# Optimization experiments

Measured on AMD Instinct MI355X. Metric: run time of the kernel, lower is better.

Reference implementation:

```python
import jax, jax.numpy as jnp
import numpy as np
from itertools import combinations

Nt, Nrf, Nk, FEAT, BATCH = 64, 4, 8, 512, 1024
Ng = Nt // Nk                      # 8
_MAX = len(list(combinations(range(Ng), Nrf)))  # 70
CSETSIZE = int(2 ** np.floor(np.log2(_MAX)))    # 64
SQRT_NRF = np.float32(np.sqrt(Nrf))


def _generate_antenna_selection_set(num_target):
    """Max-hamming-distance antenna selection set (numpy, matches torch code)."""
    combs = list(combinations(range(Ng), Nrf))
    maxSize = len(combs)
    globalSet = np.zeros((maxSize, Nt, Nrf), np.float32)
    for i, act in enumerate(combs):
        for j, a in enumerate(act):
            globalSet[i, a * Nk:a * Nk + Nk, j] = 1.0
    gsum = globalSet.sum(-1)  # (maxSize, Nt)
    selectSet = np.zeros((num_target, Nt, Nrf), np.float32)
    available = []
    for idx in range(num_target):
        if len(available) == 0:
            available = list(range(maxSize))
        if idx == 0:
            hd = np.zeros(len(available))
        else:
            sel = selectSet[:idx].sum(-1)            # (idx, Nt)
            cand = gsum[np.array(available)]          # (nAvail, Nt)
            hd = (sel[None, :, :] != cand[:, None, :]).sum(axis=(1, 2))
        sid = available[int(np.argmax(hd))]
        selectSet[idx] = globalSet[sid]
        available.remove(sid)
    return selectSet


def setup_inputs() -> dict:
    key = jax.random.key(0)
    ks = jax.random.split(key, 7)
    s = 1.0 / np.sqrt(FEAT)
    DDIM = CSETSIZE * Nrf * Nrf
    return {
        "x": jax.random.normal(ks[0], (BATCH, FEAT), jnp.float32),
        "W_A": jax.random.normal(ks[1], (Nt, FEAT), jnp.float32) * s,
        "b_A": jax.random.normal(ks[2], (Nt,), jnp.float32) * s,
        "W_Dr": jax.random.normal(ks[3], (DDIM, FEAT), jnp.float32) * s,
        "b_Dr": jax.random.normal(ks[4], (DDIM,), jnp.float32) * s,
        "W_Di": jax.random.normal(ks[5], (DDIM, FEAT), jnp.float32) * s,
        "b_Di": jax.random.normal(ks[6], (DDIM,), jnp.float32) * s,
        "CSet": jnp.asarray(_generate_antenna_selection_set(CSETSIZE)),
    }


def reference(x, W_A, b_A, W_Dr, b_Dr, W_Di, b_Di, CSet):
    B = x.shape[0]
    theta = x @ W_A.T + b_A                          # (B, Nt)
    cosT, sinT = jnp.cos(theta), jnp.sin(theta)
    eye = jnp.eye(Nt, dtype=x.dtype)
    A_real = (cosT[:, :, None] * eye)[:, None]       # (B, 1, Nt, Nt) diag-embed
    A_imag = (sinT[:, :, None] * eye)[:, None]
    D_real = (x @ W_Dr.T + b_Dr).reshape(B, CSETSIZE, Nrf, Nrf)
    D_imag = (x @ W_Di.T + b_Di).reshape(B, CSETSIZE, Nrf, Nrf)
    # diag(cos) @ C == row-scale of C (identical math to the dense matmul)
    ArC = cosT[:, None, :, None] * CSet[None]        # (B, CSetSize, Nt, Nrf)
    AiC = sinT[:, None, :, None] * CSet[None]
    ArCDr = ArC @ D_real
    ArCDi = ArC @ D_imag
    AiCDr = AiC @ D_real
    AiCDi = AiC @ D_imag
    V_real = ArCDr - AiCDi                           # (B, CSetSize, Nt, Nrf)
    V_imag = ArCDi + AiCDr
    V_F = jnp.sqrt(jnp.sum(V_real ** 2 + V_imag ** 2, axis=(2, 3)))
    V_F = V_F[:, :, None, None]
    D_real_n = SQRT_NRF * D_real / V_F
    D_imag_n = SQRT_NRF * D_imag / V_F
    return (A_real, A_imag, D_real_n, D_imag_n, CSet)
```

## Files before the change

kernel.cpp:

```cpp
#include <hip/hip_runtime.h>
#include <math.h>

#define BATCH 1024
#define FEAT  512
#define NT    64
#define DDIM  1024

typedef __attribute__((ext_vector_type(8))) short  short8;
typedef __attribute__((ext_vector_type(4))) float  floatx4;

#define AIMG_OFF  0
#define BIMG_OFF  1048576
#define THETA_OFF 3276800

__device__ __forceinline__ unsigned short bf16rne(float f) {
    unsigned int u = __float_as_uint(f);
    return (unsigned short)((u + 0x7fffu + ((u >> 16) & 1u)) >> 16);
}

__device__ __forceinline__ void gld16(const unsigned char* g, unsigned char* l) {
    __builtin_amdgcn_global_load_lds(
        (const __attribute__((address_space(1))) unsigned int*)g,
        (__attribute__((address_space(3))) unsigned int*)l, 16, 0, 0);
}

__global__ __launch_bounds__(256) void k0_convert(
    const float* __restrict__ x,
    const float* __restrict__ W_A,
    const float* __restrict__ W_Dr,
    const float* __restrict__ W_Di,
    unsigned char* __restrict__ ws)
{
    unsigned short* aimg = (unsigned short*)(ws + AIMG_OFF);
    unsigned short* bimg = (unsigned short*)(ws + BIMG_OFF);
    const int gtid = blockIdx.x * 256 + threadIdx.x;

    for (int idx = gtid; idx < 200704; idx += 65536) {
        const float* src;
        unsigned short* dst;
        if (idx < 65536) {
            const int rt = idx >> 12, kb = (idx >> 9) & 7;
            const int r  = (idx >> 3) & 63, c = idx & 7;
            src = x + ((size_t)(rt * 64 + r) * FEAT + kb * 64 + c * 8);
            dst = aimg + ((rt * 8 + kb) * 4096 + r * 64 + ((c ^ (r & 7)) * 8));
        } else {
            const int j  = idx - 65536;
            const int ct = j >> 12, kb = (j >> 9) & 7;
            const int n  = (j >> 3) & 63, c = j & 7;
            const float* wrow;
            if (ct < 32) {
                const int g = n >> 5, h = (n >> 4) & 1, pos = n & 15;
                wrow = (h ? W_Di : W_Dr) + (size_t)(ct * 32 + g * 16 + pos) * FEAT;
            } else {
                wrow = W_A + (size_t)n * FEAT;
            }
            src = wrow + kb * 64 + c * 8;
            dst = bimg + ((ct * 8 + kb) * 4096 + n * 64 + ((c ^ (n & 7)) * 8));
        }
        const float4 v0 = *(const float4*)src;
        const float4 v1 = *(const float4*)(src + 4);
        short8 o;
        o[0] = (short)bf16rne(v0.x); o[1] = (short)bf16rne(v0.y);
        o[2] = (short)bf16rne(v0.z); o[3] = (short)bf16rne(v0.w);
        o[4] = (short)bf16rne(v1.x); o[5] = (short)bf16rne(v1.y);
        o[6] = (short)bf16rne(v1.z); o[7] = (short)bf16rne(v1.w);
        *(short8*)dst = o;
    }
}

__global__ __launch_bounds__(256) void k1_gemm(
    const unsigned char* __restrict__ ws,
    const float* __restrict__ b_A,
    const float* __restrict__ b_Dr, const float* __restrict__ b_Di,
    float* __restrict__ out, float* __restrict__ theta_ws)
{
    __shared__ __align__(16) unsigned char smem[32768];

    const int bid  = blockIdx.x;
    const int rt   = bid & 15;
    const int ct   = bid >> 4;
    const int tid  = threadIdx.x;
    const int lane = tid & 63;
    const int wv   = tid >> 6;
    const int ln   = lane & 15;
    const int quad = lane >> 4;
    const int row0 = rt * 64;

    const unsigned char* Atiles = ws + AIMG_OFF + (size_t)rt * 8 * 8192;
    const unsigned char* Btiles = ws + BIMG_OFF + (size_t)ct * 8 * 8192;

    const int g0 = (wv * 2 + 0) * 1024;
    const int g1 = (wv * 2 + 1) * 1024;
    const int lo = lane * 16;

    floatx4 acc[4] = {{0,0,0,0},{0,0,0,0},{0,0,0,0},{0,0,0,0}};

    {
        unsigned char* La = smem;
        unsigned char* Lb = smem + 8192;
        gld16(Atiles + g0 + lo, La + g0);
        gld16(Atiles + g1 + lo, La + g1);
        gld16(Btiles + g0 + lo, Lb + g0);
        gld16(Btiles + g1 + lo, Lb + g1);
    }

    const int rowOffA = (wv * 16 + ln) * 128;
    const int swz = ln & 7;
    int cur = 0;

    #pragma unroll 1
    for (int kb = 0; kb < 8; ++kb) {
        __syncthreads();
        if (kb < 7) {
            const unsigned char* At = Atiles + (kb + 1) * 8192;
            const unsigned char* Bt = Btiles + (kb + 1) * 8192;
            unsigned char* La = smem + (cur ^ 1) * 16384;
            unsigned char* Lb = La + 8192;
            gld16(At + g0 + lo, La + g0);
            gld16(At + g1 + lo, La + g1);
            gld16(Bt + g0 + lo, Lb + g0);
            gld16(Bt + g1 + lo, Lb + g1);
        }
        const unsigned char* La = smem + cur * 16384;
        const unsigned char* Lb = La + 8192;
        #pragma unroll
        for (int ks = 0; ks < 2; ++ks) {
            const int ca = ((ks * 4 + quad) ^ swz) * 16;
            const short8 a = *(const short8*)(La + rowOffA + ca);
            #pragma unroll
            for (int t = 0; t < 4; ++t) {
                const short8 b = *(const short8*)(Lb + (t * 16 + ln) * 128 + ca);
                acc[t] = __builtin_amdgcn_mfma_f32_16x16x32_bf16(a, b, acc[t], 0, 0, 0);
            }
        }
        cur ^= 1;
    }

    if (ct < 32) {
        const size_t drn = (size_t)2 * BATCH * 4096;
        const size_t din = drn + (size_t)BATCH * DDIM;
        const int woff = ct * 32;
        #pragma unroll
        for (int p = 0; p < 2; ++p) {
            const int colg = woff + p * 16 + ln;
            const float br = b_Dr[colg];
            const float bi = b_Di[colg];
            float dr[4], di[4], ps[4];
            #pragma unroll
            for (int i = 0; i < 4; ++i) {
                dr[i] = acc[2 * p][i] + br;
                di[i] = acc[2 * p + 1][i] + bi;
                ps[i] = dr[i] * dr[i] + di[i] * di[i];
            }
            #pragma unroll
            for (int i = 0; i < 4; ++i) {
                ps[i] += __shfl_xor(ps[i], 1);
                ps[i] += __shfl_xor(ps[i], 2);
                ps[i] += __shfl_xor(ps[i], 4);
                ps[i] += __shfl_xor(ps[i], 8);
            }
            #pragma unroll
            for (int i = 0; i < 4; ++i) {
                const float scale = 2.0f / sqrtf(8.0f * ps[i]);
                const size_t row_g = (size_t)(row0 + wv * 16 + quad * 4 + i);
                out[drn + row_g * DDIM + colg] = dr[i] * scale;
                out[din + row_g * DDIM + colg] = di[i] * scale;
            }
        }
    } else {
        #pragma unroll
        for (int t = 0; t < 4; ++t) {
            const int colg = t * 16 + ln;
            const float ba = b_A[colg];
            #pragma unroll
            for (int i = 0; i < 4; ++i) {
                const int row_g = row0 + wv * 16 + quad * 4 + i;
                theta_ws[row_g * NT + colg] = acc[t][i] + ba;
            }
        }
    }
}

__global__ __launch_bounds__(256) void k2_fill(
    const float* __restrict__ theta_ws,
    const float* __restrict__ cset,
    float* __restrict__ out)
{
    const int beta = blockIdx.x;
    const int tid  = threadIdx.x;

    if (beta < 4096) {
        const int b  = beta >> 2;
        const int rg = beta & 3;
        const int t  = rg * 16 + (tid >> 4);
        const int j  = tid & 15;

        const float th = theta_ws[b * NT + t];
        float s, c;
        sincosf(th, &s, &c);

        float4 vr = {0.f, 0.f, 0.f, 0.f};
        float4 vi = {0.f, 0.f, 0.f, 0.f};
        if ((t >> 2) == j) {
            ((float*)&vr)[t & 3] = c;
            ((float*)&vi)[t & 3] = s;
        }
        const size_t off = (size_t)b * 4096 + t * 64 + j * 4;
        *(float4*)(out + off) = vr;
        *(float4*)(out + (size_t)BATCH * 4096 + off) = vi;
    } else {
        const int cb = beta - 4096;
        const size_t base = (size_t)2 * BATCH * 4096 + (size_t)2 * BATCH * DDIM;
        ((float4*)(out + base))[cb * 256 + tid] = ((const float4*)cset)[cb * 256 + tid];
    }
}

extern "C" void kernel_launch(void* const* d_in, const int* in_sizes, int n_in,
                              void* d_out, int out_size, void* d_ws, size_t ws_size,
                              hipStream_t stream) {
    const float* x    = (const float*)d_in[0];
    const float* W_A  = (const float*)d_in[1];
    const float* b_A  = (const float*)d_in[2];
    const float* W_Dr = (const float*)d_in[3];
    const float* b_Dr = (const float*)d_in[4];
    const float* W_Di = (const float*)d_in[5];
    const float* b_Di = (const float*)d_in[6];
    const float* CSet = (const float*)d_in[7];
    float* out = (float*)d_out;
    unsigned char* ws = (unsigned char*)d_ws;
    float* theta = (float*)(ws + THETA_OFF);

    k0_convert<<<256, 256, 0, stream>>>(x, W_A, W_Dr, W_Di, ws);
    k1_gemm<<<528, 256, 0, stream>>>(ws, b_A, b_Dr, b_Di, out, theta);
    k2_fill<<<4112, 256, 0, stream>>>(theta, CSet, out);
}
```

Baseline: 107.1 us.

## Merge three launches into two, computing theta in prep kernel and A fill in GEMM

The theta GEMM (x·W_A) moves out of the main GEMM kernel into dedicated blocks of the prep kernel, which convert x and W_A to bf16 on the fly through LDS. The CSet copy also moves into the prep kernel. The diagonal A_real/A_imag fill becomes extra blocks of the main GEMM kernel, one block per batch row with sincos computed once into shared memory. This cuts one kernel launch and its inter-kernel gap, and lets the output fill overlap with the D GEMM, at the cost of an unpipelined small GEMM sitting in the prep kernel.

After: 109.6 us. +2.4%, slower.

```diff
diff --git a/kernel.cpp b/kernel.cpp
--- a/kernel.cpp
+++ b/kernel.cpp
@@ -7,6 +7,7 @@
 #define DDIM  1024
 
 typedef __attribute__((ext_vector_type(8))) short  short8;
+typedef __attribute__((ext_vector_type(4))) short  short4v;
 typedef __attribute__((ext_vector_type(4))) float  floatx4;
 
 #define AIMG_OFF  0
@@ -16,6 +17,12 @@
 __device__ __forceinline__ unsigned short bf16rne(float f) {
     unsigned int u = __float_as_uint(f);
     return (unsigned short)((u + 0x7fffu + ((u >> 16) & 1u)) >> 16);
+}
+__device__ __forceinline__ short4v pack4(const float4 a) {
+    short4v r;
+    r[0] = (short)bf16rne(a.x); r[1] = (short)bf16rne(a.y);
+    r[2] = (short)bf16rne(a.z); r[3] = (short)bf16rne(a.w);
+    return r;
 }
 
 __device__ __forceinline__ void gld16(const unsigned char* g, unsigned char* l) {
@@ -24,119 +31,181 @@
         (__attribute__((address_space(3))) unsigned int*)l, 16, 0, 0);
 }
 
-__global__ __launch_bounds__(256) void k0_convert(
+
+__global__ __launch_bounds__(256) void k0_prep(
     const float* __restrict__ x,
-    const float* __restrict__ W_A,
-    const float* __restrict__ W_Dr,
-    const float* __restrict__ W_Di,
-    unsigned char* __restrict__ ws)
+    const float* __restrict__ W_A,  const float* __restrict__ b_A,
+    const float* __restrict__ W_Dr, const float* __restrict__ W_Di,
+    const float* __restrict__ cset,
+    unsigned char* __restrict__ ws, float* __restrict__ out)
 {
-    unsigned short* aimg = (unsigned short*)(ws + AIMG_OFF);
-    unsigned short* bimg = (unsigned short*)(ws + BIMG_OFF);
-    const int gtid = blockIdx.x * 256 + threadIdx.x;
-
-    for (int idx = gtid; idx < 200704; idx += 65536) {
-        const float* src;
-        unsigned short* dst;
-        if (idx < 65536) {
-            const int rt = idx >> 12, kb = (idx >> 9) & 7;
-            const int r  = (idx >> 3) & 63, c = idx & 7;
-            src = x + ((size_t)(rt * 64 + r) * FEAT + kb * 64 + c * 8);
-            dst = aimg + ((rt * 8 + kb) * 4096 + r * 64 + ((c ^ (r & 7)) * 8));
-        } else {
-            const int j  = idx - 65536;
-            const int ct = j >> 12, kb = (j >> 9) & 7;
-            const int n  = (j >> 3) & 63, c = j & 7;
-            const float* wrow;
-            if (ct < 32) {
+    __shared__ __align__(16) unsigned short As[64][40];
+    __shared__ __align__(16) unsigned short Bs[64][40];
+
+    const int bid = blockIdx.x;
+    const int tid = threadIdx.x;
+
+    if (bid < 256) {
+        unsigned short* aimg = (unsigned short*)(ws + AIMG_OFF);
+        unsigned short* bimg = (unsigned short*)(ws + BIMG_OFF);
+        const int gtid = bid * 256 + tid;
+        for (int idx = gtid; idx < 196608; idx += 65536) {
+            const float* src;
+            unsigned short* dst;
+            if (idx < 65536) {
+                const int rt = idx >> 12, kb = (idx >> 9) & 7;
+                const int r  = (idx >> 3) & 63, c = idx & 7;
+                src = x + ((size_t)(rt * 64 + r) * FEAT + kb * 64 + c * 8);
+                dst = aimg + ((rt * 8 + kb) * 4096 + r * 64 + ((c ^ (r & 7)) * 8));
+            } else {
+                const int j  = idx - 65536;
+                const int ct = j >> 12, kb = (j >> 9) & 7;
+                const int n  = (j >> 3) & 63, c = j & 7;
                 const int g = n >> 5, h = (n >> 4) & 1, pos = n & 15;
-                wrow = (h ? W_Di : W_Dr) + (size_t)(ct * 32 + g * 16 + pos) * FEAT;
-            } else {
-                wrow = W_A + (size_t)n * FEAT;
-            }
-            src = wrow + kb * 64 + c * 8;
-            dst = bimg + ((ct * 8 + kb) * 4096 + n * 64 + ((c ^ (n & 7)) * 8));
-        }
-        const float4 v0 = *(const float4*)src;
-        const float4 v1 = *(const float4*)(src + 4);
-        short8 o;
-        o[0] = (short)bf16rne(v0.x); o[1] = (short)bf16rne(v0.y);
-        o[2] = (short)bf16rne(v0.z); o[3] = (short)bf16rne(v0.w);
-        o[4] = (short)bf16rne(v1.x); o[5] = (short)bf16rne(v1.y);
-        o[6] = (short)bf16rne(v1.z); o[7] = (short)bf16rne(v1.w);
-        *(short8*)dst = o;
+                const float* wrow =
+                    (h ? W_Di : W_Dr) + (size_t)(ct * 32 + g * 16 + pos) * FEAT;
+                src = wrow + kb * 64 + c * 8;
+                dst = bimg + ((ct * 8 + kb) * 4096 + n * 64 + ((c ^ (n & 7)) * 8));
+            }
+            const float4 v0 = *(const float4*)src;
+            const float4 v1 = *(const float4*)(src + 4);
+            short8 o;
+            o[0] = (short)bf16rne(v0.x); o[1] = (short)bf16rne(v0.y);
+            o[2] = (short)bf16rne(v0.z); o[3] = (short)bf16rne(v0.w);
+            o[4] = (short)bf16rne(v1.x); o[5] = (short)bf16rne(v1.y);
+            o[6] = (short)bf16rne(v1.z); o[7] = (short)bf16rne(v1.w);
+            *(short8*)dst = o;
+        }
+    } else if (bid < 272) {
+        float* theta_ws = (float*)(ws + THETA_OFF);
+        const int lane = tid & 63;
+        const int wv   = tid >> 6;
+        const int ln   = lane & 15;
+        const int quad = lane >> 4;
+        const int f = tid & 7;
+        const int r = tid >> 3;
+        const int row0 = (bid - 256) * 64;
+
+        const float* arow0 = x + (size_t)(row0 + r) * FEAT;
+        const float* arow1 = x + (size_t)(row0 + r + 32) * FEAT;
+        const float* brow0 = W_A + (size_t)r * FEAT;
+        const float* brow1 = W_A + (size_t)(r + 32) * FEAT;
+
+        float4 pa0 = *(const float4*)(arow0 + f * 4);
+        float4 pa1 = *(const float4*)(arow1 + f * 4);
+        float4 pb0 = *(const float4*)(brow0 + f * 4);
+        float4 pb1 = *(const float4*)(brow1 + f * 4);
+
+        floatx4 acc[4] = {{0,0,0,0},{0,0,0,0},{0,0,0,0},{0,0,0,0}};
+
+        #pragma unroll 1
+        for (int it = 0; it < 16; ++it) {
+            __syncthreads();
+            *(short4v*)&As[r][f * 4]      = pack4(pa0);
+            *(short4v*)&As[r + 32][f * 4] = pack4(pa1);
+            *(short4v*)&Bs[r][f * 4]      = pack4(pb0);
+            *(short4v*)&Bs[r + 32][f * 4] = pack4(pb1);
+            __syncthreads();
+            if (it < 15) {
+                const int ko = (it + 1) * 32 + f * 4;
+                pa0 = *(const float4*)(arow0 + ko);
+                pa1 = *(const float4*)(arow1 + ko);
+                pb0 = *(const float4*)(brow0 + ko);
+                pb1 = *(const float4*)(brow1 + ko);
+            }
+            const short8 a = *(const short8*)&As[wv * 16 + ln][quad * 8];
+            #pragma unroll
+            for (int t = 0; t < 4; ++t) {
+                const short8 b = *(const short8*)&Bs[t * 16 + ln][quad * 8];
+                acc[t] = __builtin_amdgcn_mfma_f32_16x16x32_bf16(a, b, acc[t], 0, 0, 0);
+            }
+        }
+        #pragma unroll
+        for (int t = 0; t < 4; ++t) {
+            const int colg = t * 16 + ln;
+            const float ba = b_A[colg];
+            #pragma unroll
+            for (int i = 0; i < 4; ++i) {
+                const int row_g = row0 + wv * 16 + quad * 4 + i;
+                theta_ws[row_g * NT + colg] = acc[t][i] + ba;
+            }
+        }
+    } else {
+        const int cb = bid - 272;
+        const size_t base = (size_t)2 * BATCH * 4096 + (size_t)2 * BATCH * DDIM;
+        ((float4*)(out + base))[cb * 256 + tid] = ((const float4*)cset)[cb * 256 + tid];
     }
 }
 
-__global__ __launch_bounds__(256) void k1_gemm(
+__global__ __launch_bounds__(256) void k1_main(
     const unsigned char* __restrict__ ws,
-    const float* __restrict__ b_A,
     const float* __restrict__ b_Dr, const float* __restrict__ b_Di,
-    float* __restrict__ out, float* __restrict__ theta_ws)
+    float* __restrict__ out)
 {
     __shared__ __align__(16) unsigned char smem[32768];
 
-    const int bid  = blockIdx.x;
-    const int rt   = bid & 15;
-    const int ct   = bid >> 4;
-    const int tid  = threadIdx.x;
-    const int lane = tid & 63;
-    const int wv   = tid >> 6;
-    const int ln   = lane & 15;
-    const int quad = lane >> 4;
-    const int row0 = rt * 64;
-
-    const unsigned char* Atiles = ws + AIMG_OFF + (size_t)rt * 8 * 8192;
-    const unsigned char* Btiles = ws + BIMG_OFF + (size_t)ct * 8 * 8192;
-
-    const int g0 = (wv * 2 + 0) * 1024;
-    const int g1 = (wv * 2 + 1) * 1024;
-    const int lo = lane * 16;
-
-    floatx4 acc[4] = {{0,0,0,0},{0,0,0,0},{0,0,0,0},{0,0,0,0}};
-
-    {
-        unsigned char* La = smem;
-        unsigned char* Lb = smem + 8192;
-        gld16(Atiles + g0 + lo, La + g0);
-        gld16(Atiles + g1 + lo, La + g1);
-        gld16(Btiles + g0 + lo, Lb + g0);
-        gld16(Btiles + g1 + lo, Lb + g1);
-    }
-
-    const int rowOffA = (wv * 16 + ln) * 128;
-    const int swz = ln & 7;
-    int cur = 0;
-
-    #pragma unroll 1
-    for (int kb = 0; kb < 8; ++kb) {
-        __syncthreads();
-        if (kb < 7) {
-            const unsigned char* At = Atiles + (kb + 1) * 8192;
-            const unsigned char* Bt = Btiles + (kb + 1) * 8192;
-            unsigned char* La = smem + (cur ^ 1) * 16384;
-            unsigned char* Lb = La + 8192;
-            gld16(At + g0 + lo, La + g0);
-            gld16(At + g1 + lo, La + g1);
-            gld16(Bt + g0 + lo, Lb + g0);
-            gld16(Bt + g1 + lo, Lb + g1);
-        }
-        const unsigned char* La = smem + cur * 16384;
-        const unsigned char* Lb = La + 8192;
-        #pragma unroll
-        for (int ks = 0; ks < 2; ++ks) {
-            const int ca = ((ks * 4 + quad) ^ swz) * 16;
-            const short8 a = *(const short8*)(La + rowOffA + ca);
-            #pragma unroll
-            for (int t = 0; t < 4; ++t) {
-                const short8 b = *(const short8*)(Lb + (t * 16 + ln) * 128 + ca);
-                acc[t] = __builtin_amdgcn_mfma_f32_16x16x32_bf16(a, b, acc[t], 0, 0, 0);
-            }
-        }
-        cur ^= 1;
-    }
-
-    if (ct < 32) {
+    const int bid = blockIdx.x;
+    const int tid = threadIdx.x;
+
+    if (bid < 512) {
+        const int rt   = bid & 15;
+        const int ct   = bid >> 4;
+        const int lane = tid & 63;
+        const int wv   = tid >> 6;
+        const int ln   = lane & 15;
+        const int quad = lane >> 4;
+        const int row0 = rt * 64;
+
+        const unsigned char* Atiles = ws + AIMG_OFF + (size_t)rt * 8 * 8192;
+        const unsigned char* Btiles = ws + BIMG_OFF + (size_t)ct * 8 * 8192;
+
+        const int g0 = (wv * 2 + 0) * 1024;
+        const int g1 = (wv * 2 + 1) * 1024;
+        const int lo = lane * 16;
+
+        floatx4 acc[4] = {{0,0,0,0},{0,0,0,0},{0,0,0,0},{0,0,0,0}};
+
+        {
+            unsigned char* La = smem;
+            unsigned char* Lb = smem + 8192;
+            gld16(Atiles + g0 + lo, La + g0);
+            gld16(Atiles + g1 + lo, La + g1);
+            gld16(Btiles + g0 + lo, Lb + g0);
+            gld16(Btiles + g1 + lo, Lb + g1);
+        }
+
+        const int rowOffA = (wv * 16 + ln) * 128;
+        const int swz = ln & 7;
+        int cur = 0;
+
+        #pragma unroll 1
+        for (int kb = 0; kb < 8; ++kb) {
+            __syncthreads();
+            if (kb < 7) {
+                const unsigned char* At = Atiles + (kb + 1) * 8192;
+                const unsigned char* Bt = Btiles + (kb + 1) * 8192;
+                unsigned char* La = smem + (cur ^ 1) * 16384;
+                unsigned char* Lb = La + 8192;
+                gld16(At + g0 + lo, La + g0);
+                gld16(At + g1 + lo, La + g1);
+                gld16(Bt + g0 + lo, Lb + g0);
+                gld16(Bt + g1 + lo, Lb + g1);
+            }
+            const unsigned char* La = smem + cur * 16384;
+            const unsigned char* Lb = La + 8192;
+            #pragma unroll
+            for (int ks = 0; ks < 2; ++ks) {
+                const int ca = ((ks * 4 + quad) ^ swz) * 16;
+                const short8 a = *(const short8*)(La + rowOffA + ca);
+                #pragma unroll
+                for (int t = 0; t < 4; ++t) {
+                    const short8 b = *(const short8*)(Lb + (t * 16 + ln) * 128 + ca);
+                    acc[t] = __builtin_amdgcn_mfma_f32_16x16x32_bf16(a, b, acc[t], 0, 0, 0);
+                }
+            }
+            cur ^= 1;
+        }
+
         const size_t drn = (size_t)2 * BATCH * 4096;
         const size_t din = drn + (size_t)BATCH * DDIM;
         const int woff = ct * 32;
@@ -168,50 +237,34 @@
             }
         }
     } else {
+        const float* theta_ws = (const float*)(ws + THETA_OFF);
+        float* cosT = (float*)smem;
+        float* sinT = cosT + NT;
+        const int b = bid - 512;
+
+        if (tid < NT) {
+            float s, c;
+            sincosf(theta_ws[b * NT + tid], &s, &c);
+            cosT[tid] = c; sinT[tid] = s;
+        }
+        __syncthreads();
+
+        float* ar = out + (size_t)b * 4096;
+        float* ai = out + (size_t)BATCH * 4096 + (size_t)b * 4096;
         #pragma unroll
-        for (int t = 0; t < 4; ++t) {
-            const int colg = t * 16 + ln;
-            const float ba = b_A[colg];
-            #pragma unroll
-            for (int i = 0; i < 4; ++i) {
-                const int row_g = row0 + wv * 16 + quad * 4 + i;
-                theta_ws[row_g * NT + colg] = acc[t][i] + ba;
-            }
-        }
-    }
-}
-
-__global__ __launch_bounds__(256) void k2_fill(
-    const float* __restrict__ theta_ws,
-    const float* __restrict__ cset,
-    float* __restrict__ out)
-{
-    const int beta = blockIdx.x;
-    const int tid  = threadIdx.x;
-
-    if (beta < 4096) {
-        const int b  = beta >> 2;
-        const int rg = beta & 3;
-        const int t  = rg * 16 + (tid >> 4);
-        const int j  = tid & 15;
-
-        const float th = theta_ws[b * NT + t];
-        float s, c;
-        sincosf(th, &s, &c);
-
-        float4 vr = {0.f, 0.f, 0.f, 0.f};
-        float4 vi = {0.f, 0.f, 0.f, 0.f};
-        if ((t >> 2) == j) {
-            ((float*)&vr)[t & 3] = c;
-            ((float*)&vi)[t & 3] = s;
-        }
-        const size_t off = (size_t)b * 4096 + t * 64 + j * 4;
-        *(float4*)(out + off) = vr;
-        *(float4*)(out + (size_t)BATCH * 4096 + off) = vi;
-    } else {
-        const int cb = beta - 4096;
-        const size_t base = (size_t)2 * BATCH * 4096 + (size_t)2 * BATCH * DDIM;
-        ((float4*)(out + base))[cb * 256 + tid] = ((const float4*)cset)[cb * 256 + tid];
+        for (int it = 0; it < 4; ++it) {
+            const int idx = tid + it * 256;
+            const int tt = idx >> 4;
+            const int j0 = (idx & 15) * 4;
+            float4 vr = {0.f, 0.f, 0.f, 0.f};
+            float4 vi = {0.f, 0.f, 0.f, 0.f};
+            if (tt >= j0 && tt < j0 + 4) {
+                ((float*)&vr)[tt - j0] = cosT[tt];
+                ((float*)&vi)[tt - j0] = sinT[tt];
+            }
+            ((float4*)ar)[idx] = vr;
+            ((float4*)ai)[idx] = vi;
+        }
     }
 }
 
@@ -228,9 +281,7 @@
     const float* CSet = (const float*)d_in[7];
     float* out = (float*)d_out;
     unsigned char* ws = (unsigned char*)d_ws;
-    float* theta = (float*)(ws + THETA_OFF);
-
-    k0_convert<<<256, 256, 0, stream>>>(x, W_A, W_Dr, W_Di, ws);
-    k1_gemm<<<528, 256, 0, stream>>>(ws, b_A, b_Dr, b_Di, out, theta);
-    k2_fill<<<4112, 256, 0, stream>>>(theta, CSet, out);
-}
+
+    k0_prep<<<288, 256, 0, stream>>>(x, W_A, b_A, W_Dr, W_Di, CSet, ws, out);
+    k1_main<<<1536, 256, 0, stream>>>(ws, b_Dr, b_Di, out);
+}
```
